# Optimization experiments

Measured on AMD Instinct MI355X. Metric: run time of the kernel, lower is better.

## Reference

```python
import jax, jax.numpy as jnp
import numpy as np

B = 8192
N_INPUTS = 16 * 12 * 64  # 12288, FEATURE_FACTORIZE=False
H0, H1, H2 = 256, 32, 32
OUTPUT_SCALE = 300.0
WDL_SCALE = 200.0
AVG_ACTIVE = 30.0  # ~30 active features per position (NNUE sparsity)


def setup_inputs() -> dict:
    key = jax.random.key(0)
    ks = jax.random.split(key, 11)
    p = AVG_ACTIVE / N_INPUTS
    # near-one-hot sparse binary feature vectors, as produced by get_features()
    wf = (jax.random.uniform(ks[0], (B, N_INPUTS)) < p).astype(jnp.float32)
    bf = (jax.random.uniform(ks[1], (B, N_INPUTS)) < p).astype(jnp.float32)
    side = jax.random.randint(ks[2], (B,), 0, 2).astype(jnp.bool_)
    qs1, qs2, qs3 = float(1 << 6), float(1 << 6), float(1 << 5)
    ft_w = jax.random.normal(ks[3], (H0, N_INPUTS), jnp.float32) * jnp.sqrt(2.0 / N_INPUTS)
    ft_b = jax.random.normal(ks[4], (H0,), jnp.float32) * 0.5
    l1_w = jax.random.normal(ks[5], (H1, 2 * H0), jnp.float32) * (32.0 / qs1)
    l1_b = jax.random.normal(ks[6], (H1,), jnp.float32) * 0.5
    l2_w = jax.random.normal(ks[7], (H2, H1), jnp.float32) * (32.0 / qs2)
    l2_b = jax.random.normal(ks[8], (H2,), jnp.float32) * 0.5
    l3_w = jax.random.normal(ks[9], (1, H2), jnp.float32) * (2048.0 / (OUTPUT_SCALE * qs3))
    l3_b = jax.random.normal(ks[10], (1,), jnp.float32) * 0.5
    return {"white_features": wf, "black_features": bf, "side": side,
            "ft_w": ft_w, "ft_b": ft_b, "l1_w": l1_w, "l1_b": l1_b,
            "l2_w": l2_w, "l2_b": l2_b, "l3_w": l3_w, "l3_b": l3_b}


def reference(white_features, black_features, side, ft_w, ft_b,
              l1_w, l1_b, l2_w, l2_b, l3_w, l3_b):
    # feature transformer on each perspective: [B, H0]
    w = white_features @ ft_w.T + ft_b
    b = black_features @ ft_w.T + ft_b
    s = side[:, None]
    # side-to-move perspective first: [B, 2*H0]
    acc = jnp.where(s, jnp.concatenate([w, b], axis=1),
                    jnp.concatenate([b, w], axis=1))
    o0 = jnp.clip(acc, 0.0, 1.0)
    o1 = jnp.clip(o0 @ l1_w.T + l1_b, 0.0, 1.0)
    o2 = jnp.clip(o1 @ l2_w.T + l2_b, 0.0, 1.0)
    o3 = (o2 @ l3_w.T + l3_b) * OUTPUT_SCALE  # [B, 1]
    return jax.nn.sigmoid(o3 / WDL_SCALE)
```

## Files before the change

### kernel.cpp

```cpp
#include <hip/hip_runtime.h>
#include <math.h>

#define NB 8192
#define NI 12288
#define H0 256
#define H1 32
#define H2 32
#define MAXA 256
#define OUT_SCALE 300.0f
#define WDL_SCALE 200.0f

typedef float          f32x4 __attribute__((ext_vector_type(4)));
typedef unsigned short u16x4 __attribute__((ext_vector_type(4)));

#define FTT_B  ((size_t)NI * H0 * 2)
#define WS_NEED FTT_B

__device__ __forceinline__ unsigned short f2bf(float f) {
    unsigned u = __float_as_uint(f);
    u += 0x7FFFu + ((u >> 16) & 1u);
    return (unsigned short)(u >> 16);
}
__device__ __forceinline__ f32x4 bf4_to_f32(u16x4 h) {
    f32x4 r;
    r.x = __uint_as_float(((unsigned)h.x) << 16);
    r.y = __uint_as_float(((unsigned)h.y) << 16);
    r.z = __uint_as_float(((unsigned)h.z) << 16);
    r.w = __uint_as_float(((unsigned)h.w) << 16);
    return r;
}

__global__ __launch_bounds__(256) void nnue_ft_transpose_bf16(
    const float* __restrict__ src, unsigned short* __restrict__ dst)
{
    __shared__ float tile[64][65];
    const int bx = blockIdx.x;
    const int by = blockIdx.y;
    const int tx = threadIdx.x;
    const int ty = threadIdx.y;
    const int col = bx * 64 + tx;
    for (int j = ty; j < 64; j += 4)
        tile[j][tx] = src[(size_t)(by * 64 + j) * NI + col];
    __syncthreads();
    const int h = by * 64 + tx;
    for (int j = ty; j < 64; j += 4)
        dst[(size_t)(bx * 64 + j) * H0 + h] = f2bf(tile[tx][j]);
}

__global__ __launch_bounds__(256) void nnue_fwd(
    const float* __restrict__ wf, const float* __restrict__ bf,
    const int* __restrict__ side,
    const unsigned short* __restrict__ ftb16,
    const float* __restrict__ ft_b,
    const float* __restrict__ l1_w, const float* __restrict__ l1_b,
    const float* __restrict__ l2_w, const float* __restrict__ l2_b,
    const float* __restrict__ l3_w, const float* __restrict__ l3_b,
    float* __restrict__ out)
{
    __shared__ int   idxW[MAXA], idxB[MAXA];
    __shared__ int   cnts[2];
    __shared__ float pacc[4][2][H0] __attribute__((aligned(16)));
    __shared__ float o0[2 * H0];
    __shared__ float o1[H1];

    const int row = blockIdx.x;
    const int t   = threadIdx.x;
    if (t < 2) cnts[t] = 0;
    __syncthreads();

    const f32x4* wf4 = (const f32x4*)(wf + (size_t)row * NI);
    const f32x4* bf4 = (const f32x4*)(bf + (size_t)row * NI);

    {
        f32x4 v[12];
        #pragma unroll
        for (int k = 0; k < 12; ++k)
            v[k] = __builtin_nontemporal_load(&wf4[t + k * 256]);
        #pragma unroll
        for (int k = 0; k < 12; ++k) {
            const int base = (t + k * 256) * 4;
            int m = (v[k].x != 0.f ? 1 : 0) | (v[k].y != 0.f ? 2 : 0)
                  | (v[k].z != 0.f ? 4 : 0) | (v[k].w != 0.f ? 8 : 0);
            while (m) {
                const int b = __ffs(m) - 1;
                m &= m - 1;
                idxW[atomicAdd(&cnts[0], 1)] = base + b;
            }
        }
    }
    __syncthreads();
    const int nW = cnts[0];

    const int w = t >> 6;
    const int l = t & 63;
    const unsigned short* ftl = ftb16 + 4 * l;

    f32x4 u[12];
    #pragma unroll
    for (int k = 0; k < 12; ++k)
        u[k] = __builtin_nontemporal_load(&bf4[t + k * 256]);

    {
        f32x4 a0 = {0.f, 0.f, 0.f, 0.f}, a1 = a0;
        int i = w;
        for (; i + 4 < nW; i += 8) {
            const int i0 = __builtin_amdgcn_readfirstlane(idxW[i]);
            const int i1 = __builtin_amdgcn_readfirstlane(idxW[i + 4]);
            const u16x4 h0 = *(const u16x4*)(ftl + (size_t)i0 * H0);
            const u16x4 h1 = *(const u16x4*)(ftl + (size_t)i1 * H0);
            a0 += bf4_to_f32(h0);
            a1 += bf4_to_f32(h1);
        }
        if (i < nW) {
            const int i0 = __builtin_amdgcn_readfirstlane(idxW[i]);
            a0 += bf4_to_f32(*(const u16x4*)(ftl + (size_t)i0 * H0));
        }
        *(f32x4*)&pacc[w][0][4 * l] = a0 + a1;
    }

    #pragma unroll
    for (int k = 0; k < 12; ++k) {
        const int base = (t + k * 256) * 4;
        int m = (u[k].x != 0.f ? 1 : 0) | (u[k].y != 0.f ? 2 : 0)
              | (u[k].z != 0.f ? 4 : 0) | (u[k].w != 0.f ? 8 : 0);
        while (m) {
            const int b = __ffs(m) - 1;
            m &= m - 1;
            idxB[atomicAdd(&cnts[1], 1)] = base + b;
        }
    }
    __syncthreads();
    const int nB = cnts[1];

    {
        f32x4 b0 = {0.f, 0.f, 0.f, 0.f}, b1 = b0;
        int i = w;
        for (; i + 4 < nB; i += 8) {
            const int i0 = __builtin_amdgcn_readfirstlane(idxB[i]);
            const int i1 = __builtin_amdgcn_readfirstlane(idxB[i + 4]);
            const u16x4 h0 = *(const u16x4*)(ftl + (size_t)i0 * H0);
            const u16x4 h1 = *(const u16x4*)(ftl + (size_t)i1 * H0);
            b0 += bf4_to_f32(h0);
            b1 += bf4_to_f32(h1);
        }
        if (i < nB) {
            const int i0 = __builtin_amdgcn_readfirstlane(idxB[i]);
            b0 += bf4_to_f32(*(const u16x4*)(ftl + (size_t)i0 * H0));
        }
        *(f32x4*)&pacc[w][1][4 * l] = b0 + b1;
    }
    __syncthreads();

    const float ftb  = ft_b[t];
    const float accW = ftb + ((pacc[0][0][t] + pacc[1][0][t]) + (pacc[2][0][t] + pacc[3][0][t]));
    const float accB = ftb + ((pacc[0][1][t] + pacc[1][1][t]) + (pacc[2][1][t] + pacc[3][1][t]));
    const bool s = side[row] != 0;
    const float wv = fminf(fmaxf(accW, 0.f), 1.f);
    const float bv = fminf(fmaxf(accB, 0.f), 1.f);
    o0[t]      = s ? wv : bv;
    o0[t + H0] = s ? bv : wv;
    __syncthreads();

    {
        const int j = t >> 3, p = t & 7;
        const float* wrow = l1_w + j * (2 * H0);
        float sum = 0.f;
        #pragma unroll
        for (int m = 0; m < 64; ++m) {
            const int k = p + 8 * m;
            sum += wrow[k] * o0[k];
        }
        sum += __shfl_xor(sum, 1);
        sum += __shfl_xor(sum, 2);
        sum += __shfl_xor(sum, 4);
        if (p == 0) o1[j] = fminf(fmaxf(sum + l1_b[j], 0.f), 1.f);
    }
    __syncthreads();

    if (t < 32) {
        const float* wrow = l2_w + t * H1;
        float sum2 = 0.f;
        #pragma unroll
        for (int k = 0; k < H1; ++k) sum2 += wrow[k] * o1[k];
        const float o2v = fminf(fmaxf(sum2 + l2_b[t], 0.f), 1.f);
        float part = o2v * l3_w[t];
        part += __shfl_xor(part, 1);
        part += __shfl_xor(part, 2);
        part += __shfl_xor(part, 4);
        part += __shfl_xor(part, 8);
        part += __shfl_xor(part, 16);
        if (t == 0) {
            const float o3 = (part + l3_b[0]) * OUT_SCALE;
            out[row] = 1.f / (1.f + __expf(-o3 / WDL_SCALE));
        }
    }
}

__global__ __launch_bounds__(256) void nnue_fused_fallback(
    const float* __restrict__ wf, const float* __restrict__ bf,
    const int* __restrict__ side,
    const float* __restrict__ ft,
    const float* __restrict__ ft_b,
    const float* __restrict__ l1_w, const float* __restrict__ l1_b,
    const float* __restrict__ l2_w, const float* __restrict__ l2_b,
    const float* __restrict__ l3_w, const float* __restrict__ l3_b,
    float* __restrict__ out)
{
    __shared__ int   idxW[MAXA], idxB[MAXA];
    __shared__ int   cnts[2];
    __shared__ float o0[2 * H0];
    __shared__ float o1[H1];

    const int row = blockIdx.x;
    const int t   = threadIdx.x;
    if (t < 2) cnts[t] = 0;
    __syncthreads();

    const f32x4* wf4 = (const f32x4*)(wf + (size_t)row * NI);
    const f32x4* bf4 = (const f32x4*)(bf + (size_t)row * NI);
    const float ftb = ft_b[t];

    for (int half = 0; half < 2; ++half) {
        const f32x4* p4 = half ? bf4 : wf4;
        int* lst = half ? idxB : idxW;
        f32x4 v[12];
        #pragma unroll
        for (int k = 0; k < 12; ++k)
            v[k] = __builtin_nontemporal_load(&p4[t + k * 256]);
        #pragma unroll
        for (int k = 0; k < 12; ++k) {
            const int base = (t + k * 256) * 4;
            int m = (v[k].x != 0.f ? 1 : 0) | (v[k].y != 0.f ? 2 : 0)
                  | (v[k].z != 0.f ? 4 : 0) | (v[k].w != 0.f ? 8 : 0);
            while (m) {
                const int b = __ffs(m) - 1;
                m &= m - 1;
                lst[atomicAdd(&cnts[half], 1)] = base + b;
            }
        }
    }
    __syncthreads();

    const int nW = cnts[0], nB = cnts[1];
    float accW = ftb, accB = ftb;
    const float* ftr = ft + (size_t)t * NI;
    for (int j = 0; j < nW; ++j) accW += ftr[idxW[j]];
    for (int j = 0; j < nB; ++j) accB += ftr[idxB[j]];

    const bool s = side[row] != 0;
    const float wv = fminf(fmaxf(accW, 0.f), 1.f);
    const float bv = fminf(fmaxf(accB, 0.f), 1.f);
    o0[t]      = s ? wv : bv;
    o0[t + H0] = s ? bv : wv;
    __syncthreads();

    {
        const int j = t >> 3, p = t & 7;
        const float* wrow = l1_w + j * (2 * H0);
        float sum = 0.f;
        #pragma unroll
        for (int m = 0; m < 64; ++m) sum += wrow[p + 8 * m] * o0[p + 8 * m];
        sum += __shfl_xor(sum, 1);
        sum += __shfl_xor(sum, 2);
        sum += __shfl_xor(sum, 4);
        if (p == 0) o1[j] = fminf(fmaxf(sum + l1_b[j], 0.f), 1.f);
    }
    __syncthreads();

    if (t < 32) {
        const float* wrow = l2_w + t * H1;
        float sum2 = 0.f;
        #pragma unroll
        for (int k = 0; k < H1; ++k) sum2 += wrow[k] * o1[k];
        const float o2v = fminf(fmaxf(sum2 + l2_b[t], 0.f), 1.f);
        float part = o2v * l3_w[t];
        part += __shfl_xor(part, 1);
        part += __shfl_xor(part, 2);
        part += __shfl_xor(part, 4);
        part += __shfl_xor(part, 8);
        part += __shfl_xor(part, 16);
        if (t == 0) {
            const float o3 = (part + l3_b[0]) * OUT_SCALE;
            out[row] = 1.f / (1.f + __expf(-o3 / WDL_SCALE));
        }
    }
}

extern "C" void kernel_launch(void* const* d_in, const int* in_sizes, int n_in,
                              void* d_out, int out_size, void* d_ws, size_t ws_size,
                              hipStream_t stream) {
    const float* wf   = (const float*)d_in[0];
    const float* bf   = (const float*)d_in[1];
    const int*   side = (const int*)d_in[2];
    const float* ft_w = (const float*)d_in[3];
    const float* ft_b = (const float*)d_in[4];
    const float* l1_w = (const float*)d_in[5];
    const float* l1_b = (const float*)d_in[6];
    const float* l2_w = (const float*)d_in[7];
    const float* l2_b = (const float*)d_in[8];
    const float* l3_w = (const float*)d_in[9];
    const float* l3_b = (const float*)d_in[10];
    float*       out  = (float*)d_out;

    if (ws_size >= WS_NEED) {
        unsigned short* ftT = (unsigned short*)d_ws;
        nnue_ft_transpose_bf16<<<dim3(NI / 64, H0 / 64), dim3(64, 4), 0, stream>>>(ft_w, ftT);
        nnue_fwd<<<NB, 256, 0, stream>>>(wf, bf, side, ftT, ft_b,
                                         l1_w, l1_b, l2_w, l2_b, l3_w, l3_b, out);
    } else {
        nnue_fused_fallback<<<NB, 256, 0, stream>>>(wf, bf, side, ft_w, ft_b,
                                                    l1_w, l1_b, l2_w, l2_b,
                                                    l3_w, l3_b, out);
    }
}
```

Baseline: 165.3 us.

## Process four rows per block and prefetch next row's features across barriers

Each block now handles four batch rows in sequence. While the current row's feature-transformer gather runs, it issues the dense feature loads for the next white row and the current black row. The __syncthreads calls become a custom barrier that waits only for LDS traffic (lgkmcnt), so in-flight global loads can continue across it. This aims to hide the streaming-load latency of the very large sparse input reads. In exchange the grid has a quarter as many blocks, and more registers are live holding the prefetched vectors.

```diff
diff --git a/kernel.cpp b/kernel.cpp
--- a/kernel.cpp
+++ b/kernel.cpp
@@ -7,6 +7,7 @@
 #define H1 32
 #define H2 32
 #define MAXA 256
+#define ROWS 4
 #define OUT_SCALE 300.0f
 #define WDL_SCALE 200.0f
 
@@ -15,6 +16,9 @@
 
 #define FTT_B  ((size_t)NI * H0 * 2)
 #define WS_NEED FTT_B
+
+#define BAR() do { asm volatile("s_waitcnt lgkmcnt(0)" ::: "memory"); \
+                   __builtin_amdgcn_s_barrier(); } while (0)
 
 __device__ __forceinline__ unsigned short f2bf(float f) {
     unsigned u = __float_as_uint(f);
@@ -34,10 +38,8 @@
     const float* __restrict__ src, unsigned short* __restrict__ dst)
 {
     __shared__ float tile[64][65];
-    const int bx = blockIdx.x;
-    const int by = blockIdx.y;
-    const int tx = threadIdx.x;
-    const int ty = threadIdx.y;
+    const int bx = blockIdx.x, by = blockIdx.y;
+    const int tx = threadIdx.x, ty = threadIdx.y;
     const int col = bx * 64 + tx;
     for (int j = ty; j < 64; j += 4)
         tile[j][tx] = src[(size_t)(by * 64 + j) * NI + col];
@@ -47,7 +49,7 @@
         dst[(size_t)(bx * 64 + j) * H0 + h] = f2bf(tile[tx][j]);
 }
 
-__global__ __launch_bounds__(256) void nnue_fwd(
+__global__ __launch_bounds__(256) void nnue_fwd_pipe(
     const float* __restrict__ wf, const float* __restrict__ bf,
     const int* __restrict__ side,
     const unsigned short* __restrict__ ftb16,
@@ -58,24 +60,39 @@
     float* __restrict__ out)
 {
     __shared__ int   idxW[MAXA], idxB[MAXA];
-    __shared__ int   cnts[2];
+    __shared__ int   cnt[ROWS][2];
     __shared__ float pacc[4][2][H0] __attribute__((aligned(16)));
     __shared__ float o0[2 * H0];
     __shared__ float o1[H1];
 
-    const int row = blockIdx.x;
-    const int t   = threadIdx.x;
-    if (t < 2) cnts[t] = 0;
-    __syncthreads();
-
-    const f32x4* wf4 = (const f32x4*)(wf + (size_t)row * NI);
-    const f32x4* bf4 = (const f32x4*)(bf + (size_t)row * NI);
-
+    const int t = threadIdx.x;
+    const int w = t >> 6;
+    const int l = t & 63;
+    const int rbase = blockIdx.x * ROWS;
+    const unsigned short* ftl = ftb16 + 4 * l;
+
+    if (t < 2 * ROWS) ((int*)cnt)[t] = 0;
+
+    f32x4 v[12], u[12];
     {
-        f32x4 v[12];
+        const f32x4* s4 = (const f32x4*)(wf + (size_t)rbase * NI);
         #pragma unroll
         for (int k = 0; k < 12; ++k)
-            v[k] = __builtin_nontemporal_load(&wf4[t + k * 256]);
+            v[k] = __builtin_nontemporal_load(&s4[t + k * 256]);
+    }
+    BAR();
+
+    #pragma unroll 1
+    for (int r = 0; r < ROWS; ++r) {
+        const int row = rbase + r;
+
+        {
+            const f32x4* s4 = (const f32x4*)(bf + (size_t)row * NI);
+            #pragma unroll
+            for (int k = 0; k < 12; ++k)
+                u[k] = __builtin_nontemporal_load(&s4[t + k * 256]);
+        }
+
         #pragma unroll
         for (int k = 0; k < 12; ++k) {
             const int base = (t + k * 256) * 4;
@@ -84,114 +101,110 @@
             while (m) {
                 const int b = __ffs(m) - 1;
                 m &= m - 1;
-                idxW[atomicAdd(&cnts[0], 1)] = base + b;
-            }
-        }
-    }
-    __syncthreads();
-    const int nW = cnts[0];
-
-    const int w = t >> 6;
-    const int l = t & 63;
-    const unsigned short* ftl = ftb16 + 4 * l;
-
-    f32x4 u[12];
-    #pragma unroll
-    for (int k = 0; k < 12; ++k)
-        u[k] = __builtin_nontemporal_load(&bf4[t + k * 256]);
-
-    {
-        f32x4 a0 = {0.f, 0.f, 0.f, 0.f}, a1 = a0;
-        int i = w;
-        for (; i + 4 < nW; i += 8) {
-            const int i0 = __builtin_amdgcn_readfirstlane(idxW[i]);
-            const int i1 = __builtin_amdgcn_readfirstlane(idxW[i + 4]);
-            const u16x4 h0 = *(const u16x4*)(ftl + (size_t)i0 * H0);
-            const u16x4 h1 = *(const u16x4*)(ftl + (size_t)i1 * H0);
-            a0 += bf4_to_f32(h0);
-            a1 += bf4_to_f32(h1);
-        }
-        if (i < nW) {
-            const int i0 = __builtin_amdgcn_readfirstlane(idxW[i]);
-            a0 += bf4_to_f32(*(const u16x4*)(ftl + (size_t)i0 * H0));
-        }
-        *(f32x4*)&pacc[w][0][4 * l] = a0 + a1;
-    }
-
-    #pragma unroll
-    for (int k = 0; k < 12; ++k) {
-        const int base = (t + k * 256) * 4;
-        int m = (u[k].x != 0.f ? 1 : 0) | (u[k].y != 0.f ? 2 : 0)
-              | (u[k].z != 0.f ? 4 : 0) | (u[k].w != 0.f ? 8 : 0);
-        while (m) {
-            const int b = __ffs(m) - 1;
-            m &= m - 1;
-            idxB[atomicAdd(&cnts[1], 1)] = base + b;
-        }
-    }
-    __syncthreads();
-    const int nB = cnts[1];
-
-    {
-        f32x4 b0 = {0.f, 0.f, 0.f, 0.f}, b1 = b0;
-        int i = w;
-        for (; i + 4 < nB; i += 8) {
-            const int i0 = __builtin_amdgcn_readfirstlane(idxB[i]);
-            const int i1 = __builtin_amdgcn_readfirstlane(idxB[i + 4]);
-            const u16x4 h0 = *(const u16x4*)(ftl + (size_t)i0 * H0);
-            const u16x4 h1 = *(const u16x4*)(ftl + (size_t)i1 * H0);
-            b0 += bf4_to_f32(h0);
-            b1 += bf4_to_f32(h1);
-        }
-        if (i < nB) {
-            const int i0 = __builtin_amdgcn_readfirstlane(idxB[i]);
-            b0 += bf4_to_f32(*(const u16x4*)(ftl + (size_t)i0 * H0));
-        }
-        *(f32x4*)&pacc[w][1][4 * l] = b0 + b1;
-    }
-    __syncthreads();
-
-    const float ftb  = ft_b[t];
-    const float accW = ftb + ((pacc[0][0][t] + pacc[1][0][t]) + (pacc[2][0][t] + pacc[3][0][t]));
-    const float accB = ftb + ((pacc[0][1][t] + pacc[1][1][t]) + (pacc[2][1][t] + pacc[3][1][t]));
-    const bool s = side[row] != 0;
-    const float wv = fminf(fmaxf(accW, 0.f), 1.f);
-    const float bv = fminf(fmaxf(accB, 0.f), 1.f);
-    o0[t]      = s ? wv : bv;
-    o0[t + H0] = s ? bv : wv;
-    __syncthreads();
-
-    {
-        const int j = t >> 3, p = t & 7;
-        const float* wrow = l1_w + j * (2 * H0);
-        float sum = 0.f;
-        #pragma unroll
-        for (int m = 0; m < 64; ++m) {
-            const int k = p + 8 * m;
-            sum += wrow[k] * o0[k];
-        }
-        sum += __shfl_xor(sum, 1);
-        sum += __shfl_xor(sum, 2);
-        sum += __shfl_xor(sum, 4);
-        if (p == 0) o1[j] = fminf(fmaxf(sum + l1_b[j], 0.f), 1.f);
-    }
-    __syncthreads();
-
-    if (t < 32) {
-        const float* wrow = l2_w + t * H1;
-        float sum2 = 0.f;
-        #pragma unroll
-        for (int k = 0; k < H1; ++k) sum2 += wrow[k] * o1[k];
-        const float o2v = fminf(fmaxf(sum2 + l2_b[t], 0.f), 1.f);
-        float part = o2v * l3_w[t];
-        part += __shfl_xor(part, 1);
-        part += __shfl_xor(part, 2);
-        part += __shfl_xor(part, 4);
-        part += __shfl_xor(part, 8);
-        part += __shfl_xor(part, 16);
-        if (t == 0) {
-            const float o3 = (part + l3_b[0]) * OUT_SCALE;
-            out[row] = 1.f / (1.f + __expf(-o3 / WDL_SCALE));
+                idxW[atomicAdd(&cnt[r][0], 1)] = base + b;
+            }
+        }
+        BAR();
+
+        const int nW = cnt[r][0];
+        {
+            f32x4 a0 = {0.f, 0.f, 0.f, 0.f}, a1 = a0;
+            int i = w;
+            for (; i + 4 < nW; i += 8) {
+                const int i0 = __builtin_amdgcn_readfirstlane(idxW[i]);
+                const int i1 = __builtin_amdgcn_readfirstlane(idxW[i + 4]);
+                a0 += bf4_to_f32(*(const u16x4*)(ftl + (size_t)i0 * H0));
+                a1 += bf4_to_f32(*(const u16x4*)(ftl + (size_t)i1 * H0));
+            }
+            if (i < nW) {
+                const int i0 = __builtin_amdgcn_readfirstlane(idxW[i]);
+                a0 += bf4_to_f32(*(const u16x4*)(ftl + (size_t)i0 * H0));
+            }
+            *(f32x4*)&pacc[w][0][4 * l] = a0 + a1;
+        }
+
+        if (r + 1 < ROWS) {
+            const f32x4* s4 = (const f32x4*)(wf + (size_t)(row + 1) * NI);
+            #pragma unroll
+            for (int k = 0; k < 12; ++k)
+                v[k] = __builtin_nontemporal_load(&s4[t + k * 256]);
+        }
+
+        #pragma unroll
+        for (int k = 0; k < 12; ++k) {
+            const int base = (t + k * 256) * 4;
+            int m = (u[k].x != 0.f ? 1 : 0) | (u[k].y != 0.f ? 2 : 0)
+                  | (u[k].z != 0.f ? 4 : 0) | (u[k].w != 0.f ? 8 : 0);
+            while (m) {
+                const int b = __ffs(m) - 1;
+                m &= m - 1;
+                idxB[atomicAdd(&cnt[r][1], 1)] = base + b;
+            }
+        }
+        BAR();
+
+        const int nB = cnt[r][1];
+        {
+            f32x4 b0 = {0.f, 0.f, 0.f, 0.f}, b1 = b0;
+            int i = w;
+            for (; i + 4 < nB; i += 8) {
+                const int i0 = __builtin_amdgcn_readfirstlane(idxB[i]);
+                const int i1 = __builtin_amdgcn_readfirstlane(idxB[i + 4]);
+                b0 += bf4_to_f32(*(const u16x4*)(ftl + (size_t)i0 * H0));
+                b1 += bf4_to_f32(*(const u16x4*)(ftl + (size_t)i1 * H0));
+            }
+            if (i < nB) {
+                const int i0 = __builtin_amdgcn_readfirstlane(idxB[i]);
+                b0 += bf4_to_f32(*(const u16x4*)(ftl + (size_t)i0 * H0));
+            }
+            *(f32x4*)&pacc[w][1][4 * l] = b0 + b1;
+        }
+        BAR();
+
+        {
+            const float ftb  = ft_b[t];
+            const float accW = ftb + ((pacc[0][0][t] + pacc[1][0][t]) + (pacc[2][0][t] + pacc[3][0][t]));
+            const float accB = ftb + ((pacc[0][1][t] + pacc[1][1][t]) + (pacc[2][1][t] + pacc[3][1][t]));
+            const bool s = side[row] != 0;
+            const float wv = fminf(fmaxf(accW, 0.f), 1.f);
+            const float bv = fminf(fmaxf(accB, 0.f), 1.f);
+            o0[t]      = s ? wv : bv;
+            o0[t + H0] = s ? bv : wv;
+        }
+        BAR();
+
+        {
+            const int j = t >> 3, p = t & 7;
+            const float* wrow = l1_w + j * (2 * H0);
+            float sum = 0.f;
+            #pragma unroll
+            for (int m2 = 0; m2 < 64; ++m2) {
+                const int k = p + 8 * m2;
+                sum += wrow[k] * o0[k];
+            }
+            sum += __shfl_xor(sum, 1);
+            sum += __shfl_xor(sum, 2);
+            sum += __shfl_xor(sum, 4);
+            if (p == 0) o1[j] = fminf(fmaxf(sum + l1_b[j], 0.f), 1.f);
+        }
+        BAR();
+
+        if (t < 32) {
+            const float* wrow = l2_w + t * H1;
+            float sum2 = 0.f;
+            #pragma unroll
+            for (int k = 0; k < H1; ++k) sum2 += wrow[k] * o1[k];
+            const float o2v = fminf(fmaxf(sum2 + l2_b[t], 0.f), 1.f);
+            float part = o2v * l3_w[t];
+            part += __shfl_xor(part, 1);
+            part += __shfl_xor(part, 2);
+            part += __shfl_xor(part, 4);
+            part += __shfl_xor(part, 8);
+            part += __shfl_xor(part, 16);
+            if (t == 0) {
+                const float o3 = (part + l3_b[0]) * OUT_SCALE;
+                out[row] = 1.f / (1.f + __expf(-o3 / WDL_SCALE));
+            }
         }
     }
 }
@@ -305,8 +318,9 @@
     if (ws_size >= WS_NEED) {
         unsigned short* ftT = (unsigned short*)d_ws;
         nnue_ft_transpose_bf16<<<dim3(NI / 64, H0 / 64), dim3(64, 4), 0, stream>>>(ft_w, ftT);
-        nnue_fwd<<<NB, 256, 0, stream>>>(wf, bf, side, ftT, ft_b,
-                                         l1_w, l1_b, l2_w, l2_b, l3_w, l3_b, out);
+        nnue_fwd_pipe<<<NB / ROWS, 256, 0, stream>>>(wf, bf, side, ftT, ft_b,
+                                                     l1_w, l1_b, l2_w, l2_b,
+                                                     l3_w, l3_b, out);
     } else {
         nnue_fused_fallback<<<NB, 256, 0, stream>>>(wf, bf, side, ft_w, ft_b,
                                                     l1_w, l1_b, l2_w, l2_b,
```

Result: slower. 246.4 us (+49.1%).

## Replace atomic index compaction with per-wave ballot compaction and local gather

Applied to the files above, without the earlier changes.

Each wavefront builds its own list of active feature indices using ballot and popcount instead of shared-memory atomics into a block-wide list. This removes two block barriers and the atomic contention, and each wave accumulates only its own features with a 4-way unrolled gather. Launch bounds now request higher occupancy. Per-wave lists are capped at 96 entries, so any overflow would be silently dropped.

```diff
diff --git a/kernel.cpp b/kernel.cpp
--- a/kernel.cpp
+++ b/kernel.cpp
@@ -6,7 +6,7 @@
 #define H0 256
 #define H1 32
 #define H2 32
-#define MAXA 256
+#define SEGCAP 96
 #define OUT_SCALE 300.0f
 #define WDL_SCALE 200.0f
 
@@ -34,10 +34,8 @@
     const float* __restrict__ src, unsigned short* __restrict__ dst)
 {
     __shared__ float tile[64][65];
-    const int bx = blockIdx.x;
-    const int by = blockIdx.y;
-    const int tx = threadIdx.x;
-    const int ty = threadIdx.y;
+    const int bx = blockIdx.x, by = blockIdx.y;
+    const int tx = threadIdx.x, ty = threadIdx.y;
     const int col = bx * 64 + tx;
     for (int j = ty; j < 64; j += 4)
         tile[j][tx] = src[(size_t)(by * 64 + j) * NI + col];
@@ -47,7 +45,7 @@
         dst[(size_t)(bx * 64 + j) * H0 + h] = f2bf(tile[tx][j]);
 }
 
-__global__ __launch_bounds__(256) void nnue_fwd(
+__global__ __launch_bounds__(256, 7) void nnue_fwd(
     const float* __restrict__ wf, const float* __restrict__ bf,
     const int* __restrict__ side,
     const unsigned short* __restrict__ ftb16,
@@ -57,20 +55,22 @@
     const float* __restrict__ l3_w, const float* __restrict__ l3_b,
     float* __restrict__ out)
 {
-    __shared__ int   idxW[MAXA], idxB[MAXA];
-    __shared__ int   cnts[2];
+    __shared__ int   seg[4][2][SEGCAP];
     __shared__ float pacc[4][2][H0] __attribute__((aligned(16)));
     __shared__ float o0[2 * H0];
     __shared__ float o1[H1];
 
     const int row = blockIdx.x;
     const int t   = threadIdx.x;
-    if (t < 2) cnts[t] = 0;
-    __syncthreads();
+    const int w   = t >> 6;
+    const int l   = t & 63;
+    const unsigned short* ftl = ftb16 + 4 * l;
+    const unsigned long long ltmask = (1ull << l) - 1ull;
 
     const f32x4* wf4 = (const f32x4*)(wf + (size_t)row * NI);
     const f32x4* bf4 = (const f32x4*)(bf + (size_t)row * NI);
 
+    int nW = 0;
     {
         f32x4 v[12];
         #pragma unroll
@@ -78,22 +78,20 @@
             v[k] = __builtin_nontemporal_load(&wf4[t + k * 256]);
         #pragma unroll
         for (int k = 0; k < 12; ++k) {
-            const int base = (t + k * 256) * 4;
-            int m = (v[k].x != 0.f ? 1 : 0) | (v[k].y != 0.f ? 2 : 0)
-                  | (v[k].z != 0.f ? 4 : 0) | (v[k].w != 0.f ? 8 : 0);
-            while (m) {
-                const int b = __ffs(m) - 1;
-                m &= m - 1;
-                idxW[atomicAdd(&cnts[0], 1)] = base + b;
-            }
-        }
-    }
-    __syncthreads();
-    const int nW = cnts[0];
-
-    const int w = t >> 6;
-    const int l = t & 63;
-    const unsigned short* ftl = ftb16 + 4 * l;
+            const int ebase = (t + k * 256) * 4;
+            #define COMPW(c, val) { \
+                const bool nz = ((val) != 0.f); \
+                const unsigned long long mk = __ballot(nz); \
+                if (mk) { \
+                    const int pos = __popcll(mk & ltmask); \
+                    if (nz && nW + pos < SEGCAP) seg[w][0][nW + pos] = ebase + (c); \
+                    nW += __popcll(mk); \
+                } }
+            COMPW(0, v[k].x) COMPW(1, v[k].y) COMPW(2, v[k].z) COMPW(3, v[k].w)
+            #undef COMPW
+        }
+        if (nW > SEGCAP) nW = SEGCAP;
+    }
 
     f32x4 u[12];
     #pragma unroll
@@ -101,64 +99,73 @@
         u[k] = __builtin_nontemporal_load(&bf4[t + k * 256]);
 
     {
-        f32x4 a0 = {0.f, 0.f, 0.f, 0.f}, a1 = a0;
-        int i = w;
-        for (; i + 4 < nW; i += 8) {
-            const int i0 = __builtin_amdgcn_readfirstlane(idxW[i]);
-            const int i1 = __builtin_amdgcn_readfirstlane(idxW[i + 4]);
-            const u16x4 h0 = *(const u16x4*)(ftl + (size_t)i0 * H0);
-            const u16x4 h1 = *(const u16x4*)(ftl + (size_t)i1 * H0);
-            a0 += bf4_to_f32(h0);
-            a1 += bf4_to_f32(h1);
-        }
-        if (i < nW) {
-            const int i0 = __builtin_amdgcn_readfirstlane(idxW[i]);
+        f32x4 a0 = {0.f,0.f,0.f,0.f}, a1 = a0, a2 = a0, a3 = a0;
+        int i = 0;
+        for (; i + 4 <= nW; i += 4) {
+            const int i0 = __builtin_amdgcn_readfirstlane(seg[w][0][i]);
+            const int i1 = __builtin_amdgcn_readfirstlane(seg[w][0][i + 1]);
+            const int i2 = __builtin_amdgcn_readfirstlane(seg[w][0][i + 2]);
+            const int i3 = __builtin_amdgcn_readfirstlane(seg[w][0][i + 3]);
             a0 += bf4_to_f32(*(const u16x4*)(ftl + (size_t)i0 * H0));
-        }
-        *(f32x4*)&pacc[w][0][4 * l] = a0 + a1;
-    }
-
+            a1 += bf4_to_f32(*(const u16x4*)(ftl + (size_t)i1 * H0));
+            a2 += bf4_to_f32(*(const u16x4*)(ftl + (size_t)i2 * H0));
+            a3 += bf4_to_f32(*(const u16x4*)(ftl + (size_t)i3 * H0));
+        }
+        for (; i < nW; ++i) {
+            const int i0 = __builtin_amdgcn_readfirstlane(seg[w][0][i]);
+            a0 += bf4_to_f32(*(const u16x4*)(ftl + (size_t)i0 * H0));
+        }
+        *(f32x4*)&pacc[w][0][4 * l] = (a0 + a1) + (a2 + a3);
+    }
+
+    int nB = 0;
     #pragma unroll
     for (int k = 0; k < 12; ++k) {
-        const int base = (t + k * 256) * 4;
-        int m = (u[k].x != 0.f ? 1 : 0) | (u[k].y != 0.f ? 2 : 0)
-              | (u[k].z != 0.f ? 4 : 0) | (u[k].w != 0.f ? 8 : 0);
-        while (m) {
-            const int b = __ffs(m) - 1;
-            m &= m - 1;
-            idxB[atomicAdd(&cnts[1], 1)] = base + b;
-        }
-    }
-    __syncthreads();
-    const int nB = cnts[1];
-
-    {
-        f32x4 b0 = {0.f, 0.f, 0.f, 0.f}, b1 = b0;
-        int i = w;
-        for (; i + 4 < nB; i += 8) {
-            const int i0 = __builtin_amdgcn_readfirstlane(idxB[i]);
-            const int i1 = __builtin_amdgcn_readfirstlane(idxB[i + 4]);
-            const u16x4 h0 = *(const u16x4*)(ftl + (size_t)i0 * H0);
-            const u16x4 h1 = *(const u16x4*)(ftl + (size_t)i1 * H0);
-            b0 += bf4_to_f32(h0);
-            b1 += bf4_to_f32(h1);
-        }
-        if (i < nB) {
-            const int i0 = __builtin_amdgcn_readfirstlane(idxB[i]);
+        const int ebase = (t + k * 256) * 4;
+        #define COMPB(c, val) { \
+            const bool nz = ((val) != 0.f); \
+            const unsigned long long mk = __ballot(nz); \
+            if (mk) { \
+                const int pos = __popcll(mk & ltmask); \
+                if (nz && nB + pos < SEGCAP) seg[w][1][nB + pos] = ebase + (c); \
+                nB += __popcll(mk); \
+            } }
+        COMPB(0, u[k].x) COMPB(1, u[k].y) COMPB(2, u[k].z) COMPB(3, u[k].w)
+        #undef COMPB
+    }
+    if (nB > SEGCAP) nB = SEGCAP;
+
+    {
+        f32x4 b0 = {0.f,0.f,0.f,0.f}, b1 = b0, b2 = b0, b3 = b0;
+        int i = 0;
+        for (; i + 4 <= nB; i += 4) {
+            const int i0 = __builtin_amdgcn_readfirstlane(seg[w][1][i]);
+            const int i1 = __builtin_amdgcn_readfirstlane(seg[w][1][i + 1]);
+            const int i2 = __builtin_amdgcn_readfirstlane(seg[w][1][i + 2]);
+            const int i3 = __builtin_amdgcn_readfirstlane(seg[w][1][i + 3]);
             b0 += bf4_to_f32(*(const u16x4*)(ftl + (size_t)i0 * H0));
-        }
-        *(f32x4*)&pacc[w][1][4 * l] = b0 + b1;
-    }
-    __syncthreads();
-
-    const float ftb  = ft_b[t];
-    const float accW = ftb + ((pacc[0][0][t] + pacc[1][0][t]) + (pacc[2][0][t] + pacc[3][0][t]));
-    const float accB = ftb + ((pacc[0][1][t] + pacc[1][1][t]) + (pacc[2][1][t] + pacc[3][1][t]));
-    const bool s = side[row] != 0;
-    const float wv = fminf(fmaxf(accW, 0.f), 1.f);
-    const float bv = fminf(fmaxf(accB, 0.f), 1.f);
-    o0[t]      = s ? wv : bv;
-    o0[t + H0] = s ? bv : wv;
+            b1 += bf4_to_f32(*(const u16x4*)(ftl + (size_t)i1 * H0));
+            b2 += bf4_to_f32(*(const u16x4*)(ftl + (size_t)i2 * H0));
+            b3 += bf4_to_f32(*(const u16x4*)(ftl + (size_t)i3 * H0));
+        }
+        for (; i < nB; ++i) {
+            const int i0 = __builtin_amdgcn_readfirstlane(seg[w][1][i]);
+            b0 += bf4_to_f32(*(const u16x4*)(ftl + (size_t)i0 * H0));
+        }
+        *(f32x4*)&pacc[w][1][4 * l] = (b0 + b1) + (b2 + b3);
+    }
+    __syncthreads();
+
+    {
+        const float ftb  = ft_b[t];
+        const float accW = ftb + ((pacc[0][0][t] + pacc[1][0][t]) + (pacc[2][0][t] + pacc[3][0][t]));
+        const float accB = ftb + ((pacc[0][1][t] + pacc[1][1][t]) + (pacc[2][1][t] + pacc[3][1][t]));
+        const bool s = side[row] != 0;
+        const float wv = fminf(fmaxf(accW, 0.f), 1.f);
+        const float bv = fminf(fmaxf(accB, 0.f), 1.f);
+        o0[t]      = s ? wv : bv;
+        o0[t + H0] = s ? bv : wv;
+    }
     __syncthreads();
 
     {
@@ -166,8 +173,8 @@
         const float* wrow = l1_w + j * (2 * H0);
         float sum = 0.f;
         #pragma unroll
-        for (int m = 0; m < 64; ++m) {
-            const int k = p + 8 * m;
+        for (int m2 = 0; m2 < 64; ++m2) {
+            const int k = p + 8 * m2;
             sum += wrow[k] * o0[k];
         }
         sum += __shfl_xor(sum, 1);
@@ -206,7 +213,7 @@
     const float* __restrict__ l3_w, const float* __restrict__ l3_b,
     float* __restrict__ out)
 {
-    __shared__ int   idxW[MAXA], idxB[MAXA];
+    __shared__ int   idxW[256], idxB[256];
     __shared__ int   cnts[2];
     __shared__ float o0[2 * H0];
     __shared__ float o1[H1];
```

Result: slower. 243.5 us (+47.3%).
